# Kernel tuning notes

Measured on AMD Instinct MI355X. Metric: run time of the kernel, lower is better.

The kernel has to match this reference:

```python
import jax, jax.numpy as jnp
import numpy as np

N, D, H, E = 16384, 1024, 4096, 8

def setup_inputs() -> dict:
    key = jax.random.key(0)
    ks = jax.random.split(key, 7)
    s = 0.02
    return {
        "x": jax.random.normal(ks[0], (N, D), dtype=jnp.float32),
        "Ws": jax.random.normal(ks[1], (H, D), dtype=jnp.float32) * s,
        "bs": jax.random.normal(ks[2], (H,), dtype=jnp.float32) * s,
        "We": jax.random.normal(ks[3], (E, H, D), dtype=jnp.float32) * s,
        "be": jax.random.normal(ks[4], (E, H), dtype=jnp.float32) * s,
        "Wr": jax.random.normal(ks[5], (E, D), dtype=jnp.float32) * s,
        "br": jax.random.normal(ks[6], (E,), dtype=jnp.float32) * s,
    }

def reference(x, Ws, bs, We, be, Wr, br):
    # shared FFN: [N, H]
    shared = x @ Ws.T + bs
    # router: softmax over experts, top-1 via argmax (argmax(softmax)==argmax(logits), kept faithful)
    expert_scores = jax.nn.softmax(x @ Wr.T + br, axis=-1)  # [N, E]
    token_expert = jnp.argmax(expert_scores, axis=-1)       # [N]
    # mask-accumulate over the small fixed expert set (dense per-expert FFN as in source)
    routed = jnp.zeros_like(shared)
    num_experts = We.shape[0]
    for i in range(num_experts):
        mask = (token_expert == i).astype(shared.dtype)[:, None]  # [N, 1]
        routed = routed + mask * (x @ We[i].T + be[i])
    return shared + routed
```

## Files before the change

kernel.cpp:

```cpp
#include <hip/hip_runtime.h>
#include <stdint.h>

#define N_TOK 16384
#define DDIM  1024
#define HDIM  4096
#define NEXP  8
#define BM    256
#define MAXMT 72
#define MAXNR 5

#define GRID_R 4096
#define GRID_W 16384
#define GRID_B 128

typedef __attribute__((ext_vector_type(8))) short short8;
typedef __attribute__((ext_vector_type(4))) float f32x4;

__device__ __forceinline__ unsigned short f2b(float f) {
    union { float f; unsigned int u; } x; x.f = f;
    unsigned int r = x.u + 0x7FFFu + ((x.u >> 16) & 1u);
    return (unsigned short)(r >> 16);
}

__global__ __launch_bounds__(256)
void k_fused(const float* __restrict__ x, const float* __restrict__ Wr,
             const float* __restrict__ br, unsigned short* __restrict__ xb,
             int* __restrict__ eid,
             const float* __restrict__ Ws, const float* __restrict__ We,
             unsigned short* __restrict__ wc,
             const float* __restrict__ bs, const float* __restrict__ be,
             float* __restrict__ bc)
{
    const int bid = blockIdx.x;
    const int t = threadIdx.x;

    if (bid < GRID_R) {
        __shared__ float wr[NEXP * DDIM];
        for (int i = t; i < NEXP * DDIM / 4; i += 256)
            ((float4*)wr)[i] = ((const float4*)Wr)[i];
        __syncthreads();
        const int lane = t & 63;
        const int n = bid * 4 + (t >> 6);
        const float* xr = x + (size_t)n * DDIM;
        double acc[NEXP];
#pragma unroll
        for (int e = 0; e < NEXP; ++e) acc[e] = 0.0;
#pragma unroll
        for (int j = 0; j < 4; ++j) {
            const int d = j * 256 + lane * 4;
            float4 v = *(const float4*)(xr + d);
            unsigned long long pk =
                (unsigned long long)(f2b(v.x) | ((unsigned int)f2b(v.y) << 16)) |
                ((unsigned long long)(f2b(v.z) | ((unsigned int)f2b(v.w) << 16)) << 32);
            *(unsigned long long*)(xb + (size_t)n * DDIM + d) = pk;
#pragma unroll
            for (int e = 0; e < NEXP; ++e) {
                const float* w = wr + e * DDIM + d;
                acc[e] += (double)v.x * (double)w[0];
                acc[e] += (double)v.y * (double)w[1];
                acc[e] += (double)v.z * (double)w[2];
                acc[e] += (double)v.w * (double)w[3];
            }
        }
#pragma unroll
        for (int e = 0; e < NEXP; ++e)
#pragma unroll
            for (int off = 32; off > 0; off >>= 1)
                acc[e] += __shfl_down(acc[e], off);
        if (lane == 0) {
            double best = acc[0] + (double)br[0];
            int bi = 0;
#pragma unroll
            for (int e = 1; e < NEXP; ++e) {
                double v = acc[e] + (double)br[e];
                if (v > best) { best = v; bi = e; }
            }
            eid[n] = bi;
        }
    } else if (bid < GRID_R + GRID_W) {
        const size_t i = ((size_t)(bid - GRID_R) * 256 + t) * 8;
        const size_t hd = i & (size_t)(HDIM * DDIM - 1);
        float4 a0 = *(const float4*)(We + i);
        float4 a1 = *(const float4*)(We + i + 4);
        float4 b0 = *(const float4*)(Ws + hd);
        float4 b1 = *(const float4*)(Ws + hd + 4);
        uint4 o;
        o.x = f2b(a0.x + b0.x) | ((unsigned)f2b(a0.y + b0.y) << 16);
        o.y = f2b(a0.z + b0.z) | ((unsigned)f2b(a0.w + b0.w) << 16);
        o.z = f2b(a1.x + b1.x) | ((unsigned)f2b(a1.y + b1.y) << 16);
        o.w = f2b(a1.z + b1.z) | ((unsigned)f2b(a1.w + b1.w) << 16);
        *(uint4*)(wc + i) = o;
    } else {
        const int i = (bid - GRID_R - GRID_W) * 256 + t;
        bc[i] = bs[i & (HDIM - 1)] + be[i];
    }
}

__global__ __launch_bounds__(256)
void k_hist(const int* __restrict__ eid, int* __restrict__ counts)
{
    __shared__ int h[NEXP];
    const int t = threadIdx.x;
    if (t < NEXP) h[t] = 0;
    __syncthreads();
    atomicAdd(&h[eid[blockIdx.x * 256 + t]], 1);
    __syncthreads();
    if (t < NEXP && h[t]) atomicAdd(&counts[t * 16], h[t]);
}

__global__ __launch_bounds__(256)
void k_scatter(const int* __restrict__ eid, const int* __restrict__ counts,
               int* __restrict__ cursors, int* __restrict__ perm)
{
    __shared__ int cl[NEXP];
    __shared__ int h[NEXP];
    __shared__ int base[NEXP];
    const int t = threadIdx.x;
    if (t < NEXP) { cl[t] = counts[t * 16]; h[t] = 0; }
    __syncthreads();
    const int n = blockIdx.x * 256 + t;
    const int e = eid[n];
    int p = 0;
#pragma unroll
    for (int ee = 0; ee < NEXP; ++ee)
        if (ee < e) p += (cl[ee] + 255) >> 8;
    const int pbase = p << 8;
    const int rank = atomicAdd(&h[e], 1);
    __syncthreads();
    if (t < NEXP) base[t] = h[t] ? atomicAdd(&cursors[t * 16], h[t]) : 0;
    __syncthreads();
    perm[pbase + base[e] + rank] = n;
}

#define SBAR()   __builtin_amdgcn_s_barrier()
#define SCHED0() __builtin_amdgcn_sched_barrier(0)
#define LGKM0()  asm volatile("s_waitcnt lgkmcnt(0)" ::: "memory")

__global__ __launch_bounds__(512, 2)
void k_gemm(const unsigned short* __restrict__ X, const unsigned short* __restrict__ W,
            const float* __restrict__ bc, const int* __restrict__ perm,
            const int* __restrict__ cnt, float* __restrict__ out)
{
    __shared__ unsigned short lds[65536];
    __shared__ int   toksLDS[MAXNR][256];
    __shared__ float biasLDS[MAXNR][256];

    const int base  = blockIdx.x;
    const int tnr   = base & 15;
    const int tmB   = base >> 4;

    int ntE[NEXP]; int realM = 0;
#pragma unroll
    for (int e = 0; e < NEXP; ++e) {
        ntE[e] = (cnt[e * 16] + 255) >> 8;
        realM += ntE[e];
    }
    const int nR = (realM - tmB + 15) >> 4;
    const int T  = nR << 4;

    const int t    = threadIdx.x;
    const int lane = t & 63;
    const int wid  = t >> 6;
    const int wm   = wid >> 2;
    const int wn   = wid & 3;

    const int srow    = t >> 3;
    const int schunkE = (((t & 7) ^ (srow & 7)) << 3);
    unsigned short* dstT = lds + (t << 3);

    const int rA   = lane & 15;
    const int c0   = ((lane >> 4) << 3) ^ ((lane & 7) << 3);
    const int c1   = c0 ^ 32;
    const int aBase = ((2 + wm) << 13) + (rA << 6);
    const int bBase = ((wn >> 1) << 13) + ((wn & 1) << 12) + (rA << 6);
    const int colBase = tnr * 256 + wn * 64 + rA;

    int ePk = 0;
#pragma unroll
    for (int w = 0; w < MAXNR; ++w) {
        int ev = 0;
        if (w < nR) {
            const int tmW = tmB + (w << 4);
            int pre = 0;
#pragma unroll
            for (int e = 0; e < NEXP; ++e) {
                if (tmW >= pre) ev = e;
                pre += ntE[e];
            }
        }
        ePk |= (ev & 15) << (w << 2);
    }
    if (t < 256) {
#pragma unroll
        for (int w = 0; w < MAXNR; ++w) {
            if (w < nR) {
                toksLDS[w][t] = perm[(tmB + (w << 4)) * 256 + t];
                const int ev = (ePk >> (w << 2)) & 15;
                biasLDS[w][t] = bc[ev * HDIM + tnr * 256 + t];
            }
        }
    }
    __syncthreads();

    int tokCur[4], tokNext[4];
#pragma unroll
    for (int i = 0; i < 4; ++i) {
        int a = toksLDS[0][i * 64 + srow];
        tokCur[i] = a < 0 ? 0 : a;
        int b = (nR > 1) ? toksLDS[1][i * 64 + srow] : 0;
        tokNext[i] = b < 0 ? 0 : b;
    }

    f32x4 acc[8][4];
    {
        float bn[4];
#pragma unroll
        for (int n = 0; n < 4; ++n) bn[n] = biasLDS[0][wn * 64 + n * 16 + rA];
#pragma unroll
        for (int m = 0; m < 8; ++m)
#pragma unroll
            for (int n = 0; n < 4; ++n)
                acc[m][n] = (f32x4){bn[n], bn[n], bn[n], bn[n]};
    }
    short8 fa[8][2], fb[4][2];

    auto STAGE = [&](int sg, int tau) {
        if (sg >= (nR << 6)) return;
        const int tloc = sg >> 2;
        const int h    = sg & 3;
        const int kb   = (tloc & 15) << 6;
        unsigned short* d = dstT + ((tloc & 1) << 15) + (h << 13);
        const unsigned short *s0, *s1;
        if (h < 2) {
            const int wS = tloc >> 4;
            const int ee = (ePk >> (wS << 2)) & 15;
            const size_t r0 = (size_t)(ee * HDIM + tnr * 256 + h * 128 + srow) * DDIM
                              + schunkE + kb;
            s0 = W + r0; s1 = W + r0 + (size_t)64 * DDIM;
        } else {
            const bool nxt = (tloc >> 4) != (tau >> 4);
            const int i0 = (h - 2) << 1;
            const int ta = nxt ? tokNext[i0]     : tokCur[i0];
            const int tb = nxt ? tokNext[i0 + 1] : tokCur[i0 + 1];
            s0 = X + (size_t)ta * DDIM + schunkE + kb;
            s1 = X + (size_t)tb * DDIM + schunkE + kb;
        }
        __builtin_amdgcn_global_load_lds(
            (const __attribute__((address_space(1))) void*)s0,
            (__attribute__((address_space(3))) void*)d, 16, 0, 0);
        __builtin_amdgcn_global_load_lds(
            (const __attribute__((address_space(1))) void*)s1,
            (__attribute__((address_space(3))) void*)(d + 4096), 16, 0, 0);
    };

#define LDA(m) \
    fa[m][0] = *(const short8*)&lds[bufOff + aBase + (m)*1024 + c0]; \
    fa[m][1] = *(const short8*)&lds[bufOff + aBase + (m)*1024 + c1];
#define LDB(n) \
    fb[n][0] = *(const short8*)&lds[bufOff + bBase + (n)*1024 + c0]; \
    fb[n][1] = *(const short8*)&lds[bufOff + bBase + (n)*1024 + c1];
#define MM(m,n) \
    acc[m][n] = __builtin_amdgcn_mfma_f32_16x16x32_bf16(fa[m][0], fb[n][0], acc[m][n], 0,0,0); \
    acc[m][n] = __builtin_amdgcn_mfma_f32_16x16x32_bf16(fa[m][1], fb[n][1], acc[m][n], 0,0,0);

#pragma unroll
    for (int s = 0; s < 7; ++s) STAGE(s, 0);
    asm volatile("s_waitcnt vmcnt(6)" ::: "memory");
    SCHED0(); SBAR(); SCHED0();

    int w = 0;
#pragma unroll 1
    for (int tau = 0; tau < T; ++tau) {
        const int tt = tau & 15;
        const int bufOff = (tau & 1) << 15;
        const int sig = (tau << 2) + 7;

        LDB(0) LDB(1) LDB(2) LDB(3) LDA(0) LDA(1)
        SCHED0();
        LDA(2) LDA(3)
        SCHED0();
        LDA(4) LDA(5) LDA(6) LDA(7)
        STAGE(sig, tau);
        SCHED0();
        asm volatile("s_waitcnt lgkmcnt(12)" ::: "memory"); SCHED0();
        __builtin_amdgcn_s_setprio(1);
        MM(0,0) MM(0,1) MM(0,2) MM(0,3) MM(1,0) MM(1,1) MM(1,2) MM(1,3)
        __builtin_amdgcn_s_setprio(0); SCHED0();
        asm volatile("s_waitcnt lgkmcnt(8)" ::: "memory"); SCHED0();
        __builtin_amdgcn_s_setprio(1);
        MM(2,0) MM(2,1) MM(2,2) MM(2,3) MM(3,0) MM(3,1) MM(3,2) MM(3,3)
        __builtin_amdgcn_s_setprio(0); SCHED0();
        LGKM0(); SBAR(); SCHED0();
        STAGE(sig + 1, tau); STAGE(sig + 2, tau); STAGE(sig + 3, tau);
        SCHED0();
        __builtin_amdgcn_s_setprio(1);
        MM(4,0) MM(4,1) MM(4,2) MM(4,3) MM(5,0) MM(5,1) MM(5,2) MM(5,3)
        MM(6,0) MM(6,1) MM(6,2) MM(6,3) MM(7,0) MM(7,1) MM(7,2) MM(7,3)
        __builtin_amdgcn_s_setprio(0); SCHED0();
        if (tau < T - 2)       { asm volatile("s_waitcnt vmcnt(6)" ::: "memory"); }
        else if (tau == T - 2) { asm volatile("s_waitcnt vmcnt(0)" ::: "memory"); }
        SBAR(); SCHED0();

        if (tt == 15) {
            const int rsub = (lane >> 4) * 4;
#pragma unroll
            for (int m = 0; m < 8; ++m) {
                const int rl = wm * 128 + m * 16 + rsub;
                int tk[4];
#pragma unroll
                for (int j = 0; j < 4; ++j) tk[j] = toksLDS[w][rl + j];
#pragma unroll
                for (int n = 0; n < 4; ++n) {
                    const int col = colBase + n * 16;
#pragma unroll
                    for (int j = 0; j < 4; ++j)
                        if (tk[j] >= 0) out[(size_t)tk[j] * HDIM + col] = acc[m][n][j];
                }
            }
            if (w + 1 < nR) {
                float bn[4];
#pragma unroll
                for (int n = 0; n < 4; ++n) bn[n] = biasLDS[w + 1][wn * 64 + n * 16 + rA];
#pragma unroll
                for (int m = 0; m < 8; ++m)
#pragma unroll
                    for (int n = 0; n < 4; ++n)
                        acc[m][n] = (f32x4){bn[n], bn[n], bn[n], bn[n]};
#pragma unroll
                for (int i = 0; i < 4; ++i) tokCur[i] = tokNext[i];
                if (w + 2 < nR) {
#pragma unroll
                    for (int i = 0; i < 4; ++i) {
                        int v = toksLDS[w + 2][i * 64 + srow];
                        tokNext[i] = v < 0 ? 0 : v;
                    }
                }
            }
            ++w;
        }
    }
#undef LDA
#undef LDB
#undef MM
}

extern "C" void kernel_launch(void* const* d_in, const int* in_sizes, int n_in,
                              void* d_out, int out_size, void* d_ws, size_t ws_size,
                              hipStream_t stream)
{
    const float* x  = (const float*)d_in[0];
    const float* Ws = (const float*)d_in[1];
    const float* bs = (const float*)d_in[2];
    const float* We = (const float*)d_in[3];
    const float* be = (const float*)d_in[4];
    const float* Wr = (const float*)d_in[5];
    const float* br = (const float*)d_in[6];
    float* out = (float*)d_out;
    char* ws = (char*)d_ws;

    unsigned short* xb  = (unsigned short*)(ws + 0);
    unsigned short* wc  = (unsigned short*)(ws + 33554432);
    float*          bc  = (float*)(ws + 100663296);
    int*            eid = (int*)(ws + 100794368);
    int*            perm= (int*)(ws + 100859904);
    int*            cnt = (int*)(ws + 100933632);
    int*            cur = (int*)(ws + 100934144);

    hipMemsetAsync(perm, 0xFF, MAXMT * BM * sizeof(int), stream);
    hipMemsetAsync(cnt, 0, 1024, stream);

    k_fused<<<GRID_R + GRID_W + GRID_B, 256, 0, stream>>>(
        x, Wr, br, xb, eid, Ws, We, wc, bs, be, bc);
    k_hist<<<N_TOK / 256, 256, 0, stream>>>(eid, cnt);
    k_scatter<<<N_TOK / 256, 256, 0, stream>>>(eid, cnt, cur, perm);
    k_gemm<<<256, 512, 0, stream>>>(xb, wc, bc, perm, cnt, out);
}
```

Baseline: 271.2 us.

## Switch grouped GEMM to 32x32x16 MFMA and reorder fused prep blocks

The grouped expert GEMM moves from 16x16x32 bf16 MFMA tiles to 32x32x16 tiles. This changes the accumulator layout, the LDS fragment addressing and swizzle, and the output scatter indexing, and is meant to cut LDS fragment traffic per FLOP and raise MFMA throughput. Separately, the router blocks in the fused prep kernel move after the weight-conversion blocks and read Wr straight from global memory instead of staging it in LDS. The new fragment indexing carries correctness risk (the bOff expression is convoluted), and the larger accumulators may raise register pressure.

```diff
diff --git a/kernel.cpp b/kernel.cpp
--- a/kernel.cpp
+++ b/kernel.cpp
@@ -9,12 +9,13 @@
 #define MAXMT 72
 #define MAXNR 5
 
-#define GRID_R 4096
 #define GRID_W 16384
 #define GRID_B 128
-
-typedef __attribute__((ext_vector_type(8))) short short8;
-typedef __attribute__((ext_vector_type(4))) float f32x4;
+#define GRID_R 4096
+
+typedef __attribute__((ext_vector_type(8)))  short short8;
+typedef __attribute__((ext_vector_type(4)))  float f32x4;
+typedef __attribute__((ext_vector_type(16))) float f32x16;
 
 __device__ __forceinline__ unsigned short f2b(float f) {
     union { float f; unsigned int u; } x; x.f = f;
@@ -34,51 +35,8 @@
     const int bid = blockIdx.x;
     const int t = threadIdx.x;
 
-    if (bid < GRID_R) {
-        __shared__ float wr[NEXP * DDIM];
-        for (int i = t; i < NEXP * DDIM / 4; i += 256)
-            ((float4*)wr)[i] = ((const float4*)Wr)[i];
-        __syncthreads();
-        const int lane = t & 63;
-        const int n = bid * 4 + (t >> 6);
-        const float* xr = x + (size_t)n * DDIM;
-        double acc[NEXP];
-#pragma unroll
-        for (int e = 0; e < NEXP; ++e) acc[e] = 0.0;
-#pragma unroll
-        for (int j = 0; j < 4; ++j) {
-            const int d = j * 256 + lane * 4;
-            float4 v = *(const float4*)(xr + d);
-            unsigned long long pk =
-                (unsigned long long)(f2b(v.x) | ((unsigned int)f2b(v.y) << 16)) |
-                ((unsigned long long)(f2b(v.z) | ((unsigned int)f2b(v.w) << 16)) << 32);
-            *(unsigned long long*)(xb + (size_t)n * DDIM + d) = pk;
-#pragma unroll
-            for (int e = 0; e < NEXP; ++e) {
-                const float* w = wr + e * DDIM + d;
-                acc[e] += (double)v.x * (double)w[0];
-                acc[e] += (double)v.y * (double)w[1];
-                acc[e] += (double)v.z * (double)w[2];
-                acc[e] += (double)v.w * (double)w[3];
-            }
-        }
-#pragma unroll
-        for (int e = 0; e < NEXP; ++e)
-#pragma unroll
-            for (int off = 32; off > 0; off >>= 1)
-                acc[e] += __shfl_down(acc[e], off);
-        if (lane == 0) {
-            double best = acc[0] + (double)br[0];
-            int bi = 0;
-#pragma unroll
-            for (int e = 1; e < NEXP; ++e) {
-                double v = acc[e] + (double)br[e];
-                if (v > best) { best = v; bi = e; }
-            }
-            eid[n] = bi;
-        }
-    } else if (bid < GRID_R + GRID_W) {
-        const size_t i = ((size_t)(bid - GRID_R) * 256 + t) * 8;
+    if (bid < GRID_W) {
+        const size_t i = ((size_t)bid * 256 + t) * 8;
         const size_t hd = i & (size_t)(HDIM * DDIM - 1);
         float4 a0 = *(const float4*)(We + i);
         float4 a1 = *(const float4*)(We + i + 4);
@@ -90,9 +48,48 @@
         o.z = f2b(a1.x + b1.x) | ((unsigned)f2b(a1.y + b1.y) << 16);
         o.w = f2b(a1.z + b1.z) | ((unsigned)f2b(a1.w + b1.w) << 16);
         *(uint4*)(wc + i) = o;
+    } else if (bid < GRID_W + GRID_B) {
+        const int i = (bid - GRID_W) * 256 + t;
+        bc[i] = bs[i & (HDIM - 1)] + be[i];
     } else {
-        const int i = (bid - GRID_R - GRID_W) * 256 + t;
-        bc[i] = bs[i & (HDIM - 1)] + be[i];
+        const int lane = t & 63;
+        const int n = (bid - GRID_W - GRID_B) * 4 + (t >> 6);
+        const float* xr = x + (size_t)n * DDIM;
+        double acc[NEXP];
+#pragma unroll
+        for (int e = 0; e < NEXP; ++e) acc[e] = 0.0;
+#pragma unroll
+        for (int j = 0; j < 4; ++j) {
+            const int d = j * 256 + lane * 4;
+            float4 v = *(const float4*)(xr + d);
+            unsigned long long pk =
+                (unsigned long long)(f2b(v.x) | ((unsigned int)f2b(v.y) << 16)) |
+                ((unsigned long long)(f2b(v.z) | ((unsigned int)f2b(v.w) << 16)) << 32);
+            *(unsigned long long*)(xb + (size_t)n * DDIM + d) = pk;
+#pragma unroll
+            for (int e = 0; e < NEXP; ++e) {
+                float4 w = *(const float4*)(Wr + e * DDIM + d);
+                acc[e] += (double)v.x * (double)w.x;
+                acc[e] += (double)v.y * (double)w.y;
+                acc[e] += (double)v.z * (double)w.z;
+                acc[e] += (double)v.w * (double)w.w;
+            }
+        }
+#pragma unroll
+        for (int e = 0; e < NEXP; ++e)
+#pragma unroll
+            for (int off = 32; off > 0; off >>= 1)
+                acc[e] += __shfl_down(acc[e], off);
+        if (lane == 0) {
+            double best = acc[0] + (double)br[0];
+            int bi = 0;
+#pragma unroll
+            for (int e = 1; e < NEXP; ++e) {
+                double v = acc[e] + (double)br[e];
+                if (v > best) { best = v; bi = e; }
+            }
+            eid[n] = bi;
+        }
     }
 }
 
@@ -168,12 +165,17 @@
     const int schunkE = (((t & 7) ^ (srow & 7)) << 3);
     unsigned short* dstT = lds + (t << 3);
 
-    const int rA   = lane & 15;
-    const int c0   = ((lane >> 4) << 3) ^ ((lane & 7) << 3);
-    const int c1   = c0 ^ 32;
-    const int aBase = ((2 + wm) << 13) + (rA << 6);
-    const int bBase = ((wn >> 1) << 13) + ((wn & 1) << 12) + (rA << 6);
-    const int colBase = tnr * 256 + wn * 64 + rA;
+    const int rowL = lane & 31;
+    const int row7 = rowL & 7;
+    const int kla  = lane >> 5;
+    int kx[4];
+#pragma unroll
+    for (int ks = 0; ks < 4; ++ks) kx[ks] = (((ks << 1) + kla) ^ row7) << 3;
+    const int aOff = ((2 + wm) << 13) + (rowL << 6);
+    const int bOff = ((wn >> 1) << 13) + (((wn & 1) << 6) + rowL) << 6 > 0 ?
+                     ((wn >> 1) << 13) + ((((wn & 1) << 6) + rowL) << 6) :
+                     ((wn >> 1) << 13) + ((((wn & 1) << 6) + rowL) << 6);
+    const int colBase = tnr * 256 + wn * 64 + rowL;
 
     int ePk = 0;
 #pragma unroll
@@ -211,18 +213,16 @@
         tokNext[i] = b < 0 ? 0 : b;
     }
 
-    f32x4 acc[8][4];
+    f32x16 acc[4][2];
     {
-        float bn[4];
-#pragma unroll
-        for (int n = 0; n < 4; ++n) bn[n] = biasLDS[0][wn * 64 + n * 16 + rA];
-#pragma unroll
-        for (int m = 0; m < 8; ++m)
-#pragma unroll
-            for (int n = 0; n < 4; ++n)
-                acc[m][n] = (f32x4){bn[n], bn[n], bn[n], bn[n]};
-    }
-    short8 fa[8][2], fb[4][2];
+        float b0 = biasLDS[0][wn * 64 + rowL];
+        float b1 = biasLDS[0][wn * 64 + 32 + rowL];
+#pragma unroll
+        for (int m = 0; m < 4; ++m)
+#pragma unroll
+            for (int r = 0; r < 16; ++r) { acc[m][0][r] = b0; acc[m][1][r] = b1; }
+    }
+    short8 fa[4][4], fb[2][4];
 
     auto STAGE = [&](int sg, int tau) {
         if (sg >= (nR << 6)) return;
@@ -253,15 +253,13 @@
             (__attribute__((address_space(3))) void*)(d + 4096), 16, 0, 0);
     };
 
-#define LDA(m) \
-    fa[m][0] = *(const short8*)&lds[bufOff + aBase + (m)*1024 + c0]; \
-    fa[m][1] = *(const short8*)&lds[bufOff + aBase + (m)*1024 + c1];
-#define LDB(n) \
-    fb[n][0] = *(const short8*)&lds[bufOff + bBase + (n)*1024 + c0]; \
-    fb[n][1] = *(const short8*)&lds[bufOff + bBase + (n)*1024 + c1];
-#define MM(m,n) \
-    acc[m][n] = __builtin_amdgcn_mfma_f32_16x16x32_bf16(fa[m][0], fb[n][0], acc[m][n], 0,0,0); \
-    acc[m][n] = __builtin_amdgcn_mfma_f32_16x16x32_bf16(fa[m][1], fb[n][1], acc[m][n], 0,0,0);
+#define LDA(m,k) fa[m][k] = *(const short8*)&lds[bufOff + aOff + (m)*2048 + kx[k]];
+#define LDB(n,k) fb[n][k] = *(const short8*)&lds[bufOff + bOff + (n)*2048 + kx[k]];
+#define MM4(m,n) \
+    acc[m][n] = __builtin_amdgcn_mfma_f32_32x32x16_bf16(fa[m][0], fb[n][0], acc[m][n], 0,0,0); \
+    acc[m][n] = __builtin_amdgcn_mfma_f32_32x32x16_bf16(fa[m][1], fb[n][1], acc[m][n], 0,0,0); \
+    acc[m][n] = __builtin_amdgcn_mfma_f32_32x32x16_bf16(fa[m][2], fb[n][2], acc[m][n], 0,0,0); \
+    acc[m][n] = __builtin_amdgcn_mfma_f32_32x32x16_bf16(fa[m][3], fb[n][3], acc[m][n], 0,0,0);
 
 #pragma unroll
     for (int s = 0; s < 7; ++s) STAGE(s, 0);
@@ -275,57 +273,59 @@
         const int bufOff = (tau & 1) << 15;
         const int sig = (tau << 2) + 7;
 
-        LDB(0) LDB(1) LDB(2) LDB(3) LDA(0) LDA(1)
+        LDB(0,0) LDB(0,1) LDB(0,2) LDB(0,3)
+        LDB(1,0) LDB(1,1) LDB(1,2) LDB(1,3)
+        LDA(0,0) LDA(0,1) LDA(0,2) LDA(0,3)
         SCHED0();
-        LDA(2) LDA(3)
+        LDA(1,0) LDA(1,1) LDA(1,2) LDA(1,3)
         SCHED0();
-        LDA(4) LDA(5) LDA(6) LDA(7)
+        LDA(2,0) LDA(2,1) LDA(2,2) LDA(2,3)
+        LDA(3,0) LDA(3,1) LDA(3,2) LDA(3,3)
         STAGE(sig, tau);
         SCHED0();
         asm volatile("s_waitcnt lgkmcnt(12)" ::: "memory"); SCHED0();
         __builtin_amdgcn_s_setprio(1);
-        MM(0,0) MM(0,1) MM(0,2) MM(0,3) MM(1,0) MM(1,1) MM(1,2) MM(1,3)
+        MM4(0,0) MM4(0,1)
         __builtin_amdgcn_s_setprio(0); SCHED0();
         asm volatile("s_waitcnt lgkmcnt(8)" ::: "memory"); SCHED0();
         __builtin_amdgcn_s_setprio(1);
-        MM(2,0) MM(2,1) MM(2,2) MM(2,3) MM(3,0) MM(3,1) MM(3,2) MM(3,3)
+        MM4(1,0) MM4(1,1)
         __builtin_amdgcn_s_setprio(0); SCHED0();
         LGKM0(); SBAR(); SCHED0();
         STAGE(sig + 1, tau); STAGE(sig + 2, tau); STAGE(sig + 3, tau);
         SCHED0();
         __builtin_amdgcn_s_setprio(1);
-        MM(4,0) MM(4,1) MM(4,2) MM(4,3) MM(5,0) MM(5,1) MM(5,2) MM(5,3)
-        MM(6,0) MM(6,1) MM(6,2) MM(6,3) MM(7,0) MM(7,1) MM(7,2) MM(7,3)
+        MM4(2,0) MM4(2,1) MM4(3,0) MM4(3,1)
         __builtin_amdgcn_s_setprio(0); SCHED0();
         if (tau < T - 2)       { asm volatile("s_waitcnt vmcnt(6)" ::: "memory"); }
         else if (tau == T - 2) { asm volatile("s_waitcnt vmcnt(0)" ::: "memory"); }
         SBAR(); SCHED0();
 
         if (tt == 15) {
-            const int rsub = (lane >> 4) * 4;
-#pragma unroll
-            for (int m = 0; m < 8; ++m) {
-                const int rl = wm * 128 + m * 16 + rsub;
-                int tk[4];
-#pragma unroll
-                for (int j = 0; j < 4; ++j) tk[j] = toksLDS[w][rl + j];
-#pragma unroll
-                for (int n = 0; n < 4; ++n) {
-                    const int col = colBase + n * 16;
-#pragma unroll
-                    for (int j = 0; j < 4; ++j)
-                        if (tk[j] >= 0) out[(size_t)tk[j] * HDIM + col] = acc[m][n][j];
+            const int rHi = (lane >> 5) << 2;
+#pragma unroll
+            for (int m = 0; m < 4; ++m) {
+                int tk[16];
+#pragma unroll
+                for (int r = 0; r < 16; ++r) {
+                    const int row = (r & 3) + ((r >> 2) << 3) + rHi + wm * 128 + m * 32;
+                    tk[r] = toksLDS[w][row];
                 }
+#pragma unroll
+                for (int n = 0; n < 2; ++n) {
+                    const int col = colBase + n * 32;
+#pragma unroll
+                    for (int r = 0; r < 16; ++r)
+                        if (tk[r] >= 0) out[(size_t)tk[r] * HDIM + col] = acc[m][n][r];
+                }
             }
             if (w + 1 < nR) {
-                float bn[4];
-#pragma unroll
-                for (int n = 0; n < 4; ++n) bn[n] = biasLDS[w + 1][wn * 64 + n * 16 + rA];
-#pragma unroll
-                for (int m = 0; m < 8; ++m)
-#pragma unroll
-                    for (int n = 0; n < 4; ++n)
-                        acc[m][n] = (f32x4){bn[n], bn[n], bn[n], bn[n]};
+                const float b0 = biasLDS[w + 1][wn * 64 + rowL];
+                const float b1 = biasLDS[w + 1][wn * 64 + 32 + rowL];
+#pragma unroll
+                for (int m = 0; m < 4; ++m)
+#pragma unroll
+                    for (int r = 0; r < 16; ++r) { acc[m][0][r] = b0; acc[m][1][r] = b1; }
 #pragma unroll
                 for (int i = 0; i < 4; ++i) tokCur[i] = tokNext[i];
                 if (w + 2 < nR) {
@@ -341,7 +341,7 @@
     }
 #undef LDA
 #undef LDB
-#undef MM
+#undef MM4
 }
 
 extern "C" void kernel_launch(void* const* d_in, const int* in_sizes, int n_in,
@@ -369,7 +369,7 @@
     hipMemsetAsync(perm, 0xFF, MAXMT * BM * sizeof(int), stream);
     hipMemsetAsync(cnt, 0, 1024, stream);
 
-    k_fused<<<GRID_R + GRID_W + GRID_B, 256, 0, stream>>>(
+    k_fused<<<GRID_W + GRID_B + GRID_R, 256, 0, stream>>>(
         x, Wr, br, xb, eid, Ws, We, wc, bs, be, bc);
     k_hist<<<N_TOK / 256, 256, 0, stream>>>(eid, cnt);
     k_scatter<<<N_TOK / 256, 256, 0, stream>>>(eid, cnt, cur, perm);
```

Result: slower. 295.2 us (+8.9%).

## Fuse expert histogram into router blocks and drop shared-memory Wr staging

Applied to the files above, without the earlier changes.

Expert counting moves into the router blocks of the fused prep kernel, using a shared histogram plus global atomics, so the separate histogram kernel launch goes away. Router blocks now read Wr straight from global (cache-resident) memory instead of first copying 32KB into LDS. They are also placed after the weight-conversion blocks. This cuts a launch and the per-block LDS staging, which was heavy for these small blocks, at the cost of more global/L2 reads of Wr.

```diff
diff --git a/kernel.cpp b/kernel.cpp
--- a/kernel.cpp
+++ b/kernel.cpp
@@ -9,9 +9,9 @@
 #define MAXMT 72
 #define MAXNR 5
 
-#define GRID_R 4096
 #define GRID_W 16384
 #define GRID_B 128
+#define GRID_R 4096
 
 typedef __attribute__((ext_vector_type(8))) short short8;
 typedef __attribute__((ext_vector_type(4))) float f32x4;
@@ -25,60 +25,18 @@
 __global__ __launch_bounds__(256)
 void k_fused(const float* __restrict__ x, const float* __restrict__ Wr,
              const float* __restrict__ br, unsigned short* __restrict__ xb,
-             int* __restrict__ eid,
+             int* __restrict__ eid, int* __restrict__ counts,
              const float* __restrict__ Ws, const float* __restrict__ We,
              unsigned short* __restrict__ wc,
              const float* __restrict__ bs, const float* __restrict__ be,
              float* __restrict__ bc)
 {
+    __shared__ int h[NEXP];
     const int bid = blockIdx.x;
     const int t = threadIdx.x;
 
-    if (bid < GRID_R) {
-        __shared__ float wr[NEXP * DDIM];
-        for (int i = t; i < NEXP * DDIM / 4; i += 256)
-            ((float4*)wr)[i] = ((const float4*)Wr)[i];
-        __syncthreads();
-        const int lane = t & 63;
-        const int n = bid * 4 + (t >> 6);
-        const float* xr = x + (size_t)n * DDIM;
-        double acc[NEXP];
-#pragma unroll
-        for (int e = 0; e < NEXP; ++e) acc[e] = 0.0;
-#pragma unroll
-        for (int j = 0; j < 4; ++j) {
-            const int d = j * 256 + lane * 4;
-            float4 v = *(const float4*)(xr + d);
-            unsigned long long pk =
-                (unsigned long long)(f2b(v.x) | ((unsigned int)f2b(v.y) << 16)) |
-                ((unsigned long long)(f2b(v.z) | ((unsigned int)f2b(v.w) << 16)) << 32);
-            *(unsigned long long*)(xb + (size_t)n * DDIM + d) = pk;
-#pragma unroll
-            for (int e = 0; e < NEXP; ++e) {
-                const float* w = wr + e * DDIM + d;
-                acc[e] += (double)v.x * (double)w[0];
-                acc[e] += (double)v.y * (double)w[1];
-                acc[e] += (double)v.z * (double)w[2];
-                acc[e] += (double)v.w * (double)w[3];
-            }
-        }
-#pragma unroll
-        for (int e = 0; e < NEXP; ++e)
-#pragma unroll
-            for (int off = 32; off > 0; off >>= 1)
-                acc[e] += __shfl_down(acc[e], off);
-        if (lane == 0) {
-            double best = acc[0] + (double)br[0];
-            int bi = 0;
-#pragma unroll
-            for (int e = 1; e < NEXP; ++e) {
-                double v = acc[e] + (double)br[e];
-                if (v > best) { best = v; bi = e; }
-            }
-            eid[n] = bi;
-        }
-    } else if (bid < GRID_R + GRID_W) {
-        const size_t i = ((size_t)(bid - GRID_R) * 256 + t) * 8;
+    if (bid < GRID_W) {
+        const size_t i = ((size_t)bid * 256 + t) * 8;
         const size_t hd = i & (size_t)(HDIM * DDIM - 1);
         float4 a0 = *(const float4*)(We + i);
         float4 a1 = *(const float4*)(We + i + 4);
@@ -90,22 +48,54 @@
         o.z = f2b(a1.x + b1.x) | ((unsigned)f2b(a1.y + b1.y) << 16);
         o.w = f2b(a1.z + b1.z) | ((unsigned)f2b(a1.w + b1.w) << 16);
         *(uint4*)(wc + i) = o;
+    } else if (bid < GRID_W + GRID_B) {
+        const int i = (bid - GRID_W) * 256 + t;
+        bc[i] = bs[i & (HDIM - 1)] + be[i];
     } else {
-        const int i = (bid - GRID_R - GRID_W) * 256 + t;
-        bc[i] = bs[i & (HDIM - 1)] + be[i];
-    }
-}
-
-__global__ __launch_bounds__(256)
-void k_hist(const int* __restrict__ eid, int* __restrict__ counts)
-{
-    __shared__ int h[NEXP];
-    const int t = threadIdx.x;
-    if (t < NEXP) h[t] = 0;
-    __syncthreads();
-    atomicAdd(&h[eid[blockIdx.x * 256 + t]], 1);
-    __syncthreads();
-    if (t < NEXP && h[t]) atomicAdd(&counts[t * 16], h[t]);
+        if (t < NEXP) h[t] = 0;
+        __syncthreads();
+        const int lane = t & 63;
+        const int n = (bid - GRID_W - GRID_B) * 4 + (t >> 6);
+        const float* xr = x + (size_t)n * DDIM;
+        double acc[NEXP];
+#pragma unroll
+        for (int e = 0; e < NEXP; ++e) acc[e] = 0.0;
+#pragma unroll
+        for (int j = 0; j < 4; ++j) {
+            const int d = j * 256 + lane * 4;
+            float4 v = *(const float4*)(xr + d);
+            unsigned long long pk =
+                (unsigned long long)(f2b(v.x) | ((unsigned int)f2b(v.y) << 16)) |
+                ((unsigned long long)(f2b(v.z) | ((unsigned int)f2b(v.w) << 16)) << 32);
+            *(unsigned long long*)(xb + (size_t)n * DDIM + d) = pk;
+#pragma unroll
+            for (int e = 0; e < NEXP; ++e) {
+                float4 w = *(const float4*)(Wr + e * DDIM + d);
+                acc[e] += (double)v.x * (double)w.x;
+                acc[e] += (double)v.y * (double)w.y;
+                acc[e] += (double)v.z * (double)w.z;
+                acc[e] += (double)v.w * (double)w.w;
+            }
+        }
+#pragma unroll
+        for (int e = 0; e < NEXP; ++e)
+#pragma unroll
+            for (int off = 32; off > 0; off >>= 1)
+                acc[e] += __shfl_down(acc[e], off);
+        if (lane == 0) {
+            double best = acc[0] + (double)br[0];
+            int bi = 0;
+#pragma unroll
+            for (int e = 1; e < NEXP; ++e) {
+                double v = acc[e] + (double)br[e];
+                if (v > best) { best = v; bi = e; }
+            }
+            eid[n] = bi;
+            atomicAdd(&h[bi], 1);
+        }
+        __syncthreads();
+        if (t < NEXP && h[t]) atomicAdd(&counts[t * 16], h[t]);
+    }
 }
 
 __global__ __launch_bounds__(256)
@@ -369,9 +359,8 @@
     hipMemsetAsync(perm, 0xFF, MAXMT * BM * sizeof(int), stream);
     hipMemsetAsync(cnt, 0, 1024, stream);
 
-    k_fused<<<GRID_R + GRID_W + GRID_B, 256, 0, stream>>>(
-        x, Wr, br, xb, eid, Ws, We, wc, bs, be, bc);
-    k_hist<<<N_TOK / 256, 256, 0, stream>>>(eid, cnt);
+    k_fused<<<GRID_W + GRID_B + GRID_R, 256, 0, stream>>>(
+        x, Wr, br, xb, eid, cnt, Ws, We, wc, bs, be, bc);
     k_scatter<<<N_TOK / 256, 256, 0, stream>>>(eid, cnt, cur, perm);
     k_gemm<<<256, 512, 0, stream>>>(xb, wc, bc, perm, cnt, out);
 }
```

Measured after the change: 275.6 us. No clear change (+1.6%).
